# Kernel optimization log

Measured on AMD Instinct MI355X. Metric: run time of the kernel, lower is better.

## Reference

```python
import jax, jax.numpy as jnp
import numpy as np


def setup_inputs() -> dict:
    key = jax.random.key(0)
    k1, k2, k3 = jax.random.split(key, 3)
    N = 100000
    E = 1600000
    d = 128
    indices = jax.random.randint(k1, (2, E), 0, N, dtype=jnp.int64)
    values = jax.random.uniform(k2, (E,), dtype=jnp.float32)
    b = jax.random.normal(k3, (N, d), dtype=jnp.float32)
    return {"indices": indices, "values": values, "b": b, "N": N, "layer_id": 0}


def reference(indices, values, b, N, layer_id):
    # Sparse COO matmul: out[r] = sum_{e: row[e]==r} values[e] * b[col[e]]
    row = indices[0]  # [E]
    col = indices[1]  # [E]
    contrib = values[:, None] * b[col]  # [E, d] gathered + scaled edge messages
    out = jax.ops.segment_sum(contrib, row, num_segments=N)  # [N, d]
    return out
```

## Files before the change

kernel.cpp:

```cpp
#include <hip/hip_runtime.h>


#define DIM 128
#define RPB 32
#define BLK 128
#define STAGE 768
#define CAP (STAGE + 7 * RPB)
#define NCH 256
#define MAXNB 4096

__device__ __forceinline__ unsigned short f2bf(float f) {
    unsigned u = __float_as_uint(f);
    return (unsigned short)((u + 0x7FFFu + ((u >> 16) & 1u)) >> 16);
}
__device__ __forceinline__ float2 ldbf2(const char* p) {
    ushort2 h = *reinterpret_cast<const ushort2*>(p);
    float2 r;
    r.x = __uint_as_float((unsigned)h.x << 16);
    r.y = __uint_as_float((unsigned)h.y << 16);
    return r;
}

__global__ __launch_bounds__(256) void conv_kernel(
    const float* __restrict__ b, unsigned short* __restrict__ bh, int n4)
{
    for (int i = blockIdx.x * blockDim.x + threadIdx.x; i < n4;
         i += gridDim.x * blockDim.x) {
        float4 v = reinterpret_cast<const float4*>(b)[i];
        ushort4 h;
        h.x = f2bf(v.x); h.y = f2bf(v.y); h.z = f2bf(v.z); h.w = f2bf(v.w);
        reinterpret_cast<ushort4*>(bh)[i] = h;
    }
}

__global__ __launch_bounds__(256) void spmm_atomic_kernel(
    const int* __restrict__ rows, const int* __restrict__ cols,
    const float* __restrict__ vals, const float* __restrict__ b,
    float* __restrict__ out, int E)
{
    long long t = (long long)blockIdx.x * blockDim.x + threadIdx.x;
    int e = (int)(t >> 5);
    if (e >= E) return;
    int j = ((int)t & 31) * 4;
    int r = rows[e]; int c = cols[e]; float v = vals[e];
    const float4 bv = *reinterpret_cast<const float4*>(b + (size_t)c * DIM + j);
    float* o = out + (size_t)r * DIM + j;
    atomicAdd(o + 0, v * bv.x);
    atomicAdd(o + 1, v * bv.y);
    atomicAdd(o + 2, v * bv.z);
    atomicAdd(o + 3, v * bv.w);
}

__global__ __launch_bounds__(256) void coarse_count_kernel(
    const int* __restrict__ rows, int* __restrict__ ccount, int E)
{
    __shared__ int hist[MAXNB];
    for (int i = threadIdx.x; i < MAXNB; i += 256) hist[i] = 0;
    __syncthreads();
    int chunk = (E + NCH - 1) / NCH;
    int s = blockIdx.x * chunk;
    int e = min(s + chunk, E);
    for (int i = s + threadIdx.x; i < e; i += 256)
        atomicAdd(&hist[rows[i] >> 5], 1);
    __syncthreads();
    for (int i = threadIdx.x; i < MAXNB; i += 256)
        if (hist[i]) atomicAdd(&ccount[i], hist[i]);
}

__global__ __launch_bounds__(1024) void coarse_scan_kernel(
    const int* __restrict__ ccount, int* __restrict__ coffsets,
    int* __restrict__ ccursor, int NB, int E)
{
    __shared__ int s[1024];
    int t = threadIdx.x;
    int i0 = 4 * t;
    int a0 = (i0     < NB) ? ccount[i0]     : 0;
    int a1 = (i0 + 1 < NB) ? ccount[i0 + 1] : 0;
    int a2 = (i0 + 2 < NB) ? ccount[i0 + 2] : 0;
    int a3 = (i0 + 3 < NB) ? ccount[i0 + 3] : 0;
    int sum4 = a0 + a1 + a2 + a3;
    s[t] = sum4;
    __syncthreads();
    for (int off = 1; off < 1024; off <<= 1) {
        int x = (t >= off) ? s[t - off] : 0;
        __syncthreads();
        s[t] += x;
        __syncthreads();
    }
    int excl = s[t] - sum4;
    if (i0     < NB) { coffsets[i0]     = excl;                ccursor[i0]     = excl; }
    if (i0 + 1 < NB) { coffsets[i0 + 1] = excl + a0;           ccursor[i0 + 1] = excl + a0; }
    if (i0 + 2 < NB) { coffsets[i0 + 2] = excl + a0 + a1;      ccursor[i0 + 2] = excl + a0 + a1; }
    if (i0 + 3 < NB) { coffsets[i0 + 3] = excl + a0 + a1 + a2; ccursor[i0 + 3] = excl + a0 + a1 + a2; }
    if (t == 0) coffsets[NB] = E;
}

__global__ __launch_bounds__(256) void partition_kernel(
    const int* __restrict__ rows, const int* __restrict__ cols,
    const float* __restrict__ vals, int* __restrict__ ccursor,
    unsigned long long* __restrict__ pairs, int E)
{
    __shared__ int hist[MAXNB];
    __shared__ int base[MAXNB];
    for (int i = threadIdx.x; i < MAXNB; i += 256) hist[i] = 0;
    __syncthreads();
    int chunk = (E + NCH - 1) / NCH;
    int s = blockIdx.x * chunk;
    int e = min(s + chunk, E);
    for (int i = s + threadIdx.x; i < e; i += 256)
        atomicAdd(&hist[rows[i] >> 5], 1);
    __syncthreads();
    for (int i = threadIdx.x; i < MAXNB; i += 256) {
        int c = hist[i];
        base[i] = c ? atomicAdd(&ccursor[i], c) : 0;
        hist[i] = 0;
    }
    __syncthreads();
    for (int i = s + threadIdx.x; i < e; i += 256) {
        int r = rows[i];
        int cb = r >> 5;
        int pos = base[cb] + atomicAdd(&hist[cb], 1);
        unsigned long long p =
            ((unsigned long long)(unsigned)__float_as_int(vals[i]) << 32) |
            (unsigned)((cols[i] << 5) | (r & (RPB - 1)));
        pairs[pos] = p;
    }
}

template<bool BF16>
__global__ __launch_bounds__(BLK) void bucket_accum_kernel(
    const int* __restrict__ coffsets,
    const unsigned long long* __restrict__ pairs,
    const void* __restrict__ bmat, float* __restrict__ out, int N)
{
    __shared__ int2 svec[CAP];
    __shared__ int fcnt[RPB];
    __shared__ int foff[RPB + 1];
    __shared__ int stmp[RPB];

    int cb = blockIdx.x;
    int cstart = coffsets[cb];
    int Mtot = coffsets[cb + 1] - cstart;
    int M = min(Mtot, STAGE);
    int t = threadIdx.x;

    unsigned long long ep0 = 0, ep1 = 0, ep2 = 0, ep3 = 0, ep4 = 0, ep5 = 0;
    {
        const unsigned long long* p = pairs + cstart;
        if (t         < M) ep0 = p[t];
        if (t + 128   < M) ep1 = p[t + 128];
        if (t + 256   < M) ep2 = p[t + 256];
        if (t + 384   < M) ep3 = p[t + 384];
        if (t + 512   < M) ep4 = p[t + 512];
        if (t + 640   < M) ep5 = p[t + 640];
    }
    for (int i = t; i < CAP; i += BLK) svec[i] = make_int2(0, 0);
    if (t < RPB) fcnt[t] = 0;
    __syncthreads();

    if (t         < M) atomicAdd(&fcnt[(int)(ep0 & (RPB - 1))], 1);
    if (t + 128   < M) atomicAdd(&fcnt[(int)(ep1 & (RPB - 1))], 1);
    if (t + 256   < M) atomicAdd(&fcnt[(int)(ep2 & (RPB - 1))], 1);
    if (t + 384   < M) atomicAdd(&fcnt[(int)(ep3 & (RPB - 1))], 1);
    if (t + 512   < M) atomicAdd(&fcnt[(int)(ep4 & (RPB - 1))], 1);
    if (t + 640   < M) atomicAdd(&fcnt[(int)(ep5 & (RPB - 1))], 1);
    __syncthreads();

    int pc = 0;
    if (t < RPB) { pc = (fcnt[t] + 7) & ~7; stmp[t] = pc; }
    __syncthreads();
    for (int off = 1; off < RPB; off <<= 1) {
        int x = 0;
        if (t < RPB && t >= off) x = stmp[t - off];
        __syncthreads();
        if (t < RPB) stmp[t] += x;
        __syncthreads();
    }
    if (t < RPB) {
        int excl = stmp[t] - pc;
        foff[t] = excl;
        fcnt[t] = excl;
    }
    if (t == RPB - 1) foff[RPB] = stmp[t];
    __syncthreads();

#define RANK_WRITE(EP, OFS)                                                  \
    if (t + (OFS) < M) {                                                     \
        unsigned lo = (unsigned)(EP & 0xffffffffu);                          \
        int pos = atomicAdd(&fcnt[(int)(lo & (RPB - 1))], 1);                \
        svec[pos] = make_int2((int)((lo & 0xffffffe0u) << (BF16 ? 3 : 4)),   \
                              (int)(EP >> 32));                              \
    }
    RANK_WRITE(ep0, 0)   RANK_WRITE(ep1, 128) RANK_WRITE(ep2, 256)
    RANK_WRITE(ep3, 384) RANK_WRITE(ep4, 512) RANK_WRITE(ep5, 640)
#undef RANK_WRITE
    __syncthreads();

    int wid  = t >> 6;
    int lane = t & 63;
    const char* bl = (const char*)bmat + lane * (BF16 ? 4 : 8);

#define GATHER(DST, OFS)                                                     \
    if constexpr (BF16) DST = ldbf2(bl + (OFS));                             \
    else DST = *reinterpret_cast<const float2*>(bl + (OFS));

    for (int j = 0; j < 16; ++j) {
        int rl = wid * 16 + j;
        int rg = cb * RPB + rl;
        if (rg >= N) break;
        float2 acc = make_float2(0.f, 0.f);
        int ks = foff[rl], ke = foff[rl + 1];
        if (ks < ke) {
            int2 e0 = svec[ks],     e1 = svec[ks + 1];
            int2 e2 = svec[ks + 2], e3 = svec[ks + 3];
            int2 e4 = svec[ks + 4], e5 = svec[ks + 5];
            int2 e6 = svec[ks + 6], e7 = svec[ks + 7];
            float2 c0, c1, c2, c3, c4, c5, c6, c7;
            GATHER(c0, e0.x) GATHER(c1, e1.x) GATHER(c2, e2.x) GATHER(c3, e3.x)
            GATHER(c4, e4.x) GATHER(c5, e5.x) GATHER(c6, e6.x) GATHER(c7, e7.x)
            for (int k = ks + 8; k < ke; k += 8) {
                int2 f0 = svec[k],     f1 = svec[k + 1];
                int2 f2 = svec[k + 2], f3 = svec[k + 3];
                int2 f4 = svec[k + 4], f5 = svec[k + 5];
                int2 f6 = svec[k + 6], f7 = svec[k + 7];
                float2 d0, d1, d2, d3, d4, d5, d6, d7;
                GATHER(d0, f0.x) GATHER(d1, f1.x) GATHER(d2, f2.x) GATHER(d3, f3.x)
                GATHER(d4, f4.x) GATHER(d5, f5.x) GATHER(d6, f6.x) GATHER(d7, f7.x)
                __builtin_amdgcn_sched_barrier(0);
                float v;
                v = __int_as_float(e0.y); acc.x = fmaf(v, c0.x, acc.x); acc.y = fmaf(v, c0.y, acc.y);
                v = __int_as_float(e1.y); acc.x = fmaf(v, c1.x, acc.x); acc.y = fmaf(v, c1.y, acc.y);
                v = __int_as_float(e2.y); acc.x = fmaf(v, c2.x, acc.x); acc.y = fmaf(v, c2.y, acc.y);
                v = __int_as_float(e3.y); acc.x = fmaf(v, c3.x, acc.x); acc.y = fmaf(v, c3.y, acc.y);
                v = __int_as_float(e4.y); acc.x = fmaf(v, c4.x, acc.x); acc.y = fmaf(v, c4.y, acc.y);
                v = __int_as_float(e5.y); acc.x = fmaf(v, c5.x, acc.x); acc.y = fmaf(v, c5.y, acc.y);
                v = __int_as_float(e6.y); acc.x = fmaf(v, c6.x, acc.x); acc.y = fmaf(v, c6.y, acc.y);
                v = __int_as_float(e7.y); acc.x = fmaf(v, c7.x, acc.x); acc.y = fmaf(v, c7.y, acc.y);
                e0 = f0; e1 = f1; e2 = f2; e3 = f3;
                e4 = f4; e5 = f5; e6 = f6; e7 = f7;
                c0 = d0; c1 = d1; c2 = d2; c3 = d3;
                c4 = d4; c5 = d5; c6 = d6; c7 = d7;
            }
            float v;
            v = __int_as_float(e0.y); acc.x = fmaf(v, c0.x, acc.x); acc.y = fmaf(v, c0.y, acc.y);
            v = __int_as_float(e1.y); acc.x = fmaf(v, c1.x, acc.x); acc.y = fmaf(v, c1.y, acc.y);
            v = __int_as_float(e2.y); acc.x = fmaf(v, c2.x, acc.x); acc.y = fmaf(v, c2.y, acc.y);
            v = __int_as_float(e3.y); acc.x = fmaf(v, c3.x, acc.x); acc.y = fmaf(v, c3.y, acc.y);
            v = __int_as_float(e4.y); acc.x = fmaf(v, c4.x, acc.x); acc.y = fmaf(v, c4.y, acc.y);
            v = __int_as_float(e5.y); acc.x = fmaf(v, c5.x, acc.x); acc.y = fmaf(v, c5.y, acc.y);
            v = __int_as_float(e6.y); acc.x = fmaf(v, c6.x, acc.x); acc.y = fmaf(v, c6.y, acc.y);
            v = __int_as_float(e7.y); acc.x = fmaf(v, c7.x, acc.x); acc.y = fmaf(v, c7.y, acc.y);
        }
        for (int q = STAGE; q < Mtot; ++q) {
            unsigned long long p = pairs[cstart + q];
            if ((int)(p & (RPB - 1)) == rl) {
                unsigned lo = (unsigned)(p & 0xffffffffu);
                float v = __int_as_float((int)(p >> 32));
                float2 bv;
                GATHER(bv, (int)((lo & 0xffffffe0u) << (BF16 ? 3 : 4)))
                acc.x = fmaf(v, bv.x, acc.x);  acc.y = fmaf(v, bv.y, acc.y);
            }
        }
        *reinterpret_cast<float2*>(out + (size_t)rg * DIM + lane * 2) = acc;
    }
#undef GATHER
}

extern "C" void kernel_launch(void* const* d_in, const int* in_sizes, int n_in,
                              void* d_out, int out_size, void* d_ws, size_t ws_size,
                              hipStream_t stream)
{
    const int*   indices = (const int*)d_in[0];
    const float* vals    = (const float*)d_in[1];
    const float* b       = (const float*)d_in[2];
    float*       out     = (float*)d_out;

    const int E = in_sizes[1];
    const int N = in_sizes[2] / DIM;
    const int* rows = indices;
    const int* cols = indices + E;

    const int NB = (N + RPB - 1) / RPB;

    size_t pairs_bytes = (size_t)E * 8;
    size_t bh_bytes    = (size_t)N * DIM * 2;
    size_t cnt_bytes   = ((size_t)NB * 3 + 1) * 4;
    size_t needed_f32  = pairs_bytes + cnt_bytes;
    size_t needed_bf16 = pairs_bytes + bh_bytes + cnt_bytes;

    if (ws_size < needed_f32 || NB > MAXNB || NB < 1 || E < 1) {
        hipMemsetAsync(d_out, 0, (size_t)out_size * sizeof(float), stream);
        if (E >= 1) {
            const long long total = (long long)E * 32;
            const int grid = (int)((total + 255) / 256);
            spmm_atomic_kernel<<<grid, 256, 0, stream>>>(rows, cols, vals, b, out, E);
        }
        return;
    }

    const bool use_bf16 = (ws_size >= needed_bf16);

    char* base = (char*)d_ws;
    unsigned long long* pairs = (unsigned long long*)base;
    size_t off = pairs_bytes;
    unsigned short* bh = nullptr;
    if (use_bf16) { bh = (unsigned short*)(base + off); off += bh_bytes; }
    int* ccount   = (int*)(base + off);
    int* coffsets = ccount + NB;
    int* ccursor  = coffsets + (NB + 1);

    if (use_bf16)
        conv_kernel<<<2048, 256, 0, stream>>>(b, bh, N * DIM / 4);

    hipMemsetAsync(ccount, 0, (size_t)NB * sizeof(int), stream);
    coarse_count_kernel<<<NCH, 256, 0, stream>>>(rows, ccount, E);
    coarse_scan_kernel<<<1, 1024, 0, stream>>>(ccount, coffsets, ccursor, NB, E);
    partition_kernel<<<NCH, 256, 0, stream>>>(rows, cols, vals, ccursor, pairs, E);
    if (use_bf16)
        bucket_accum_kernel<true><<<NB, BLK, 0, stream>>>(coffsets, pairs, bh, out, N);
    else
        bucket_accum_kernel<false><<<NB, BLK, 0, stream>>>(coffsets, pairs, b, out, N);
}
```

Measured before the change: 155.9 us.

## Fuse bf16 conversion into count kernel and gather with half-wave split rows

The standalone bf16 conversion kernel is merged into the coarse count kernel, so one launch is removed and the conversion runs on NCH=256 blocks instead of 2048. In the accumulate kernel each wave now splits into two half-waves. Each lane loads 4 features (8-byte bf16 or 16-byte fp32) and the two halves handle alternating edges. The partial sums are combined with a cross-half shuffle before a float4 store. This widens per-lane loads and halves the gather instructions per edge, at the cost of a shuffle reduction and leaving half the lanes idle in the overflow loop.

```diff
diff --git a/kernel.cpp b/kernel.cpp
--- a/kernel.cpp
+++ b/kernel.cpp
@@ -13,24 +13,14 @@
     unsigned u = __float_as_uint(f);
     return (unsigned short)((u + 0x7FFFu + ((u >> 16) & 1u)) >> 16);
 }
-__device__ __forceinline__ float2 ldbf2(const char* p) {
-    ushort2 h = *reinterpret_cast<const ushort2*>(p);
-    float2 r;
+__device__ __forceinline__ float4 ldbf4(const char* p) {
+    ushort4 h = *reinterpret_cast<const ushort4*>(p);
+    float4 r;
     r.x = __uint_as_float((unsigned)h.x << 16);
     r.y = __uint_as_float((unsigned)h.y << 16);
+    r.z = __uint_as_float((unsigned)h.z << 16);
+    r.w = __uint_as_float((unsigned)h.w << 16);
     return r;
-}
-
-__global__ __launch_bounds__(256) void conv_kernel(
-    const float* __restrict__ b, unsigned short* __restrict__ bh, int n4)
-{
-    for (int i = blockIdx.x * blockDim.x + threadIdx.x; i < n4;
-         i += gridDim.x * blockDim.x) {
-        float4 v = reinterpret_cast<const float4*>(b)[i];
-        ushort4 h;
-        h.x = f2bf(v.x); h.y = f2bf(v.y); h.z = f2bf(v.z); h.w = f2bf(v.w);
-        reinterpret_cast<ushort4*>(bh)[i] = h;
-    }
 }
 
 __global__ __launch_bounds__(256) void spmm_atomic_kernel(
@@ -51,9 +41,17 @@
     atomicAdd(o + 3, v * bv.w);
 }
 
-__global__ __launch_bounds__(256) void coarse_count_kernel(
+__global__ __launch_bounds__(256) void conv_count_kernel(
+    const float* __restrict__ b, unsigned short* __restrict__ bh, int n4,
     const int* __restrict__ rows, int* __restrict__ ccount, int E)
 {
+    for (int i = blockIdx.x * blockDim.x + threadIdx.x; i < n4;
+         i += gridDim.x * blockDim.x) {
+        float4 v = reinterpret_cast<const float4*>(b)[i];
+        ushort4 h;
+        h.x = f2bf(v.x); h.y = f2bf(v.y); h.z = f2bf(v.z); h.w = f2bf(v.w);
+        reinterpret_cast<ushort4*>(bh)[i] = h;
+    }
     __shared__ int hist[MAXNB];
     for (int i = threadIdx.x; i < MAXNB; i += 256) hist[i] = 0;
     __syncthreads();
@@ -198,71 +196,63 @@
 
     int wid  = t >> 6;
     int lane = t & 63;
-    const char* bl = (const char*)bmat + lane * (BF16 ? 4 : 8);
+    int h    = lane >> 5;
+    int sub  = lane & 31;
+    const char* blh = (const char*)bmat + sub * (BF16 ? 8 : 16);
 
 #define GATHER(DST, OFS)                                                     \
-    if constexpr (BF16) DST = ldbf2(bl + (OFS));                             \
-    else DST = *reinterpret_cast<const float2*>(bl + (OFS));
+    if constexpr (BF16) DST = ldbf4(blh + (OFS));                            \
+    else DST = *reinterpret_cast<const float4*>(blh + (OFS));
+
+#define FMA4(EV, CV)                                                         \
+    { float v = __int_as_float(EV.y);                                        \
+      acc.x = fmaf(v, CV.x, acc.x); acc.y = fmaf(v, CV.y, acc.y);            \
+      acc.z = fmaf(v, CV.z, acc.z); acc.w = fmaf(v, CV.w, acc.w); }
 
     for (int j = 0; j < 16; ++j) {
         int rl = wid * 16 + j;
         int rg = cb * RPB + rl;
         if (rg >= N) break;
-        float2 acc = make_float2(0.f, 0.f);
+        float4 acc = make_float4(0.f, 0.f, 0.f, 0.f);
         int ks = foff[rl], ke = foff[rl + 1];
         if (ks < ke) {
-            int2 e0 = svec[ks],     e1 = svec[ks + 1];
-            int2 e2 = svec[ks + 2], e3 = svec[ks + 3];
-            int2 e4 = svec[ks + 4], e5 = svec[ks + 5];
-            int2 e6 = svec[ks + 6], e7 = svec[ks + 7];
-            float2 c0, c1, c2, c3, c4, c5, c6, c7;
+            int2 e0 = svec[ks + h],     e1 = svec[ks + 2 + h];
+            int2 e2 = svec[ks + 4 + h], e3 = svec[ks + 6 + h];
+            float4 c0, c1, c2, c3;
             GATHER(c0, e0.x) GATHER(c1, e1.x) GATHER(c2, e2.x) GATHER(c3, e3.x)
-            GATHER(c4, e4.x) GATHER(c5, e5.x) GATHER(c6, e6.x) GATHER(c7, e7.x)
             for (int k = ks + 8; k < ke; k += 8) {
-                int2 f0 = svec[k],     f1 = svec[k + 1];
-                int2 f2 = svec[k + 2], f3 = svec[k + 3];
-                int2 f4 = svec[k + 4], f5 = svec[k + 5];
-                int2 f6 = svec[k + 6], f7 = svec[k + 7];
-                float2 d0, d1, d2, d3, d4, d5, d6, d7;
+                int2 f0 = svec[k + h],     f1 = svec[k + 2 + h];
+                int2 f2 = svec[k + 4 + h], f3 = svec[k + 6 + h];
+                float4 d0, d1, d2, d3;
                 GATHER(d0, f0.x) GATHER(d1, f1.x) GATHER(d2, f2.x) GATHER(d3, f3.x)
-                GATHER(d4, f4.x) GATHER(d5, f5.x) GATHER(d6, f6.x) GATHER(d7, f7.x)
                 __builtin_amdgcn_sched_barrier(0);
-                float v;
-                v = __int_as_float(e0.y); acc.x = fmaf(v, c0.x, acc.x); acc.y = fmaf(v, c0.y, acc.y);
-                v = __int_as_float(e1.y); acc.x = fmaf(v, c1.x, acc.x); acc.y = fmaf(v, c1.y, acc.y);
-                v = __int_as_float(e2.y); acc.x = fmaf(v, c2.x, acc.x); acc.y = fmaf(v, c2.y, acc.y);
-                v = __int_as_float(e3.y); acc.x = fmaf(v, c3.x, acc.x); acc.y = fmaf(v, c3.y, acc.y);
-                v = __int_as_float(e4.y); acc.x = fmaf(v, c4.x, acc.x); acc.y = fmaf(v, c4.y, acc.y);
-                v = __int_as_float(e5.y); acc.x = fmaf(v, c5.x, acc.x); acc.y = fmaf(v, c5.y, acc.y);
-                v = __int_as_float(e6.y); acc.x = fmaf(v, c6.x, acc.x); acc.y = fmaf(v, c6.y, acc.y);
-                v = __int_as_float(e7.y); acc.x = fmaf(v, c7.x, acc.x); acc.y = fmaf(v, c7.y, acc.y);
+                FMA4(e0, c0) FMA4(e1, c1) FMA4(e2, c2) FMA4(e3, c3)
                 e0 = f0; e1 = f1; e2 = f2; e3 = f3;
-                e4 = f4; e5 = f5; e6 = f6; e7 = f7;
                 c0 = d0; c1 = d1; c2 = d2; c3 = d3;
-                c4 = d4; c5 = d5; c6 = d6; c7 = d7;
             }
-            float v;
-            v = __int_as_float(e0.y); acc.x = fmaf(v, c0.x, acc.x); acc.y = fmaf(v, c0.y, acc.y);
-            v = __int_as_float(e1.y); acc.x = fmaf(v, c1.x, acc.x); acc.y = fmaf(v, c1.y, acc.y);
-            v = __int_as_float(e2.y); acc.x = fmaf(v, c2.x, acc.x); acc.y = fmaf(v, c2.y, acc.y);
-            v = __int_as_float(e3.y); acc.x = fmaf(v, c3.x, acc.x); acc.y = fmaf(v, c3.y, acc.y);
-            v = __int_as_float(e4.y); acc.x = fmaf(v, c4.x, acc.x); acc.y = fmaf(v, c4.y, acc.y);
-            v = __int_as_float(e5.y); acc.x = fmaf(v, c5.x, acc.x); acc.y = fmaf(v, c5.y, acc.y);
-            v = __int_as_float(e6.y); acc.x = fmaf(v, c6.x, acc.x); acc.y = fmaf(v, c6.y, acc.y);
-            v = __int_as_float(e7.y); acc.x = fmaf(v, c7.x, acc.x); acc.y = fmaf(v, c7.y, acc.y);
+            FMA4(e0, c0) FMA4(e1, c1) FMA4(e2, c2) FMA4(e3, c3)
         }
-        for (int q = STAGE; q < Mtot; ++q) {
-            unsigned long long p = pairs[cstart + q];
-            if ((int)(p & (RPB - 1)) == rl) {
-                unsigned lo = (unsigned)(p & 0xffffffffu);
-                float v = __int_as_float((int)(p >> 32));
-                float2 bv;
-                GATHER(bv, (int)((lo & 0xffffffe0u) << (BF16 ? 3 : 4)))
-                acc.x = fmaf(v, bv.x, acc.x);  acc.y = fmaf(v, bv.y, acc.y);
+        if (h == 0) {
+            for (int q = STAGE; q < Mtot; ++q) {
+                unsigned long long p = pairs[cstart + q];
+                if ((int)(p & (RPB - 1)) == rl) {
+                    unsigned lo = (unsigned)(p & 0xffffffffu);
+                    float v = __int_as_float((int)(p >> 32));
+                    float4 bv;
+                    GATHER(bv, (int)((lo & 0xffffffe0u) << (BF16 ? 3 : 4)))
+                    acc.x = fmaf(v, bv.x, acc.x); acc.y = fmaf(v, bv.y, acc.y);
+                    acc.z = fmaf(v, bv.z, acc.z); acc.w = fmaf(v, bv.w, acc.w);
+                }
             }
         }
-        *reinterpret_cast<float2*>(out + (size_t)rg * DIM + lane * 2) = acc;
-    }
+        acc.x += __shfl_xor(acc.x, 32);
+        acc.y += __shfl_xor(acc.y, 32);
+        acc.z += __shfl_xor(acc.z, 32);
+        acc.w += __shfl_xor(acc.w, 32);
+        if (h == 0)
+            *reinterpret_cast<float4*>(out + (size_t)rg * DIM + sub * 4) = acc;
+    }
+#undef FMA4
 #undef GATHER
 }
 
@@ -309,11 +299,9 @@
     int* coffsets = ccount + NB;
     int* ccursor  = coffsets + (NB + 1);
 
-    if (use_bf16)
-        conv_kernel<<<2048, 256, 0, stream>>>(b, bh, N * DIM / 4);
-
     hipMemsetAsync(ccount, 0, (size_t)NB * sizeof(int), stream);
-    coarse_count_kernel<<<NCH, 256, 0, stream>>>(rows, ccount, E);
+    conv_count_kernel<<<NCH, 256, 0, stream>>>(
+        b, bh, use_bf16 ? N * DIM / 4 : 0, rows, ccount, E);
     coarse_scan_kernel<<<1, 1024, 0, stream>>>(ccount, coffsets, ccursor, NB, E);
     partition_kernel<<<NCH, 256, 0, stream>>>(rows, cols, vals, ccursor, pairs, E);
     if (use_bf16)
```

New measurement: 152.3 us. 1.02x faster.
